# Kernel tuning notes

Hardware: AMD Instinct MI355X
Metric: run time of the kernel (lower is better)

Reference implementation:

```python
import jax, jax.numpy as jnp
import numpy as np

B, D = 8192, 128
MARGIN = 0.1
N_CLASSES, N_GROUPS = 64, 8


def setup_inputs() -> dict:
    key = jax.random.key(0)
    k1, k2, k3 = jax.random.split(key, 3)
    embeddings = jax.random.normal(k1, (B, D), dtype=jnp.float32)
    labels = jax.random.randint(k2, (B,), 0, N_CLASSES, dtype=jnp.int64)
    groups = jax.random.randint(k3, (B,), 0, N_GROUPS, dtype=jnp.int64)
    return {"embeddings": embeddings, "labels": labels, "groups": groups}


def reference(embeddings, labels, groups):
    # cosine metric: L2-normalize rows (torch F.normalize eps=1e-12)
    norm = jnp.maximum(jnp.linalg.norm(embeddings, axis=1, keepdims=True), 1e-12)
    x = embeddings / norm
    dist = 1.0 - jnp.matmul(x, x.T)                      # [B, B]

    n = embeddings.shape[0]
    eye = jnp.eye(n, dtype=bool)
    same_label = labels[:, None] == labels[None, :]       # [B, B]
    pos_mask = same_label & ~eye
    neg_mask = ~same_label
    neg_sg_mask = neg_mask & (groups[:, None] == groups[None, :])

    BIG = jnp.float32(1e9)
    # hardest positive per row (masked max), hardest negative per row (masked min)
    dist_ap = jnp.max(jnp.where(pos_mask, dist, -BIG), axis=1)
    dist_an_sg = jnp.min(jnp.where(neg_sg_mask, dist, BIG), axis=1)
    dist_an_all = jnp.min(jnp.where(neg_mask, dist, BIG), axis=1)

    has_pos = jnp.any(pos_mask, axis=1)
    has_neg_sg = jnp.any(neg_sg_mask, axis=1)
    has_neg = jnp.any(neg_mask, axis=1)

    # fallback: same-group negatives preferred, else any negative
    dist_an = jnp.where(has_neg_sg, dist_an_sg, dist_an_all)

    loss = jax.nn.relu(dist_ap - dist_an + MARGIN)        # [B]
    # original only averages strictly-positive losses over valid anchors
    include = has_pos & has_neg & (loss > 0)
    cnt = jnp.sum(include.astype(jnp.float32))
    total = jnp.sum(jnp.where(include, loss, 0.0))
    final = jnp.where(cnt > 0, total / jnp.maximum(cnt, 1.0), 0.0)
    final = jnp.where(jnp.isnan(final), 0.0, final)
    return final
```

## Files before the change

### kernel.cpp

```cpp
#include <hip/hip_runtime.h>
#include <math.h>

#define NB 8192
#define DK 128
#define TI 128
#define NTILES (NB / TI)
#define NBLK (NTILES * (NTILES + 1) / 2)
#define JT 64
#define NT (TI / JT)
#define BSTRH 136
#define NCOMB (NB / 256)

typedef __attribute__((ext_vector_type(8))) short short8;
typedef __attribute__((ext_vector_type(16))) float float16;

__device__ inline unsigned short f2bf(float f) {
    unsigned int x = __float_as_uint(f);
    unsigned int r = (x + 0x7fffu + ((x >> 16) & 1u)) >> 16;
    return (unsigned short)r;
}

__global__ void norm_kernel(const float* __restrict__ emb, const int* __restrict__ labels,
                            const int* __restrict__ groups, unsigned short* __restrict__ xnb,
                            int* __restrict__ meta, float* __restrict__ accum,
                            int* __restrict__ ticket) {
    int row  = blockIdx.x * 4 + (threadIdx.x >> 6);
    int lane = threadIdx.x & 63;
    float2 v = ((const float2*)(emb + (size_t)row * DK))[lane];
    float ss = v.x * v.x + v.y * v.y;
#pragma unroll
    for (int off = 32; off; off >>= 1) ss += __shfl_xor(ss, off, 64);
    float inv = 1.0f / fmaxf(sqrtf(ss), 1e-12f);
    ushort2 o;
    o.x = f2bf(v.x * inv);
    o.y = f2bf(v.y * inv);
    ((ushort2*)(xnb + (size_t)row * DK))[lane] = o;
    if (lane == 0) meta[row] = (labels[row] << 8) | groups[row];
    if (blockIdx.x == 0 && threadIdx.x == 0) {
        accum[0] = 0.0f; accum[1] = 0.0f; ticket[0] = 0;
    }
}

__global__ __launch_bounds__(256, 3) void mine_tri(
    const unsigned short* __restrict__ xnb, const int* __restrict__ meta,
    float2* __restrict__ part) {
    __shared__ unsigned short Bs[2][JT * BSTRH];

    int bid = blockIdx.x;
    int ti = 0;
    while (bid >= NTILES - ti) { bid -= NTILES - ti; ti++; }
    const int tj = ti + bid;

    const int tid  = threadIdx.x;
    const int w    = tid >> 6;
    const int lane = tid & 63;
    const int half = lane >> 5;
    const int l31  = lane & 31;
    const int i0    = ti * TI;
    const int jbase = tj * TI;
    const int irow  = i0 + w * 32;

    short8 afrag[8];
#pragma unroll
    for (int ks = 0; ks < 8; ks++)
        afrag[ks] = *(const short8*)(xnb + (size_t)(irow + l31) * DK + ks * 16 + half * 8);

    int metaI[16];
    float apn[16], anc[16];
#pragma unroll
    for (int reg = 0; reg < 16; reg++) {
        int r = (reg & 3) + 8 * (reg >> 2) + 4 * half;
        metaI[reg] = meta[irow + r];
        apn[reg] = -1e9f; anc[reg] = -1e9f;
    }
    float apnC[4], ancC[4];
#pragma unroll
    for (int q = 0; q < 4; q++) { apnC[q] = -1e9f; ancC[q] = -1e9f; }

#pragma unroll
    for (int s = 0; s < 4; s++) {
        int chunk = tid + s * 256;
        int row = chunk >> 4, k4 = chunk & 15;
        *(uint4*)&Bs[0][row * BSTRH + k4 * 8] =
            *(const uint4*)(xnb + (size_t)(jbase + row) * DK + k4 * 8);
    }
    __syncthreads();

#pragma unroll
    for (int jt = 0; jt < NT; jt++) {
        const int cur = jt & 1;
        const int j0  = jbase + jt * JT;

        uint4 pre[4];
        if (jt + 1 < NT) {
            const int j0n = j0 + JT;
#pragma unroll
            for (int s = 0; s < 4; s++) {
                int chunk = tid + s * 256;
                int row = chunk >> 4, k4 = chunk & 15;
                pre[s] = *(const uint4*)(xnb + (size_t)(j0n + row) * DK + k4 * 8);
            }
        }

        int mjc[2];
        mjc[0] = meta[j0 + l31];
        mjc[1] = meta[j0 + 32 + l31];

#pragma unroll
        for (int ct = 0; ct < 2; ct++) {
            float16 c;
#pragma unroll
            for (int e = 0; e < 16; e++) c[e] = 0.0f;

            const int bro = ct * 32 + l31;
#pragma unroll
            for (int ks = 0; ks < 8; ks++) {
                short8 b = *(const short8*)&Bs[cur][bro * BSTRH + ks * 16 + half * 8];
                c = __builtin_amdgcn_mfma_f32_32x32x16_bf16(afrag[ks], b, c, 0, 0, 0);
            }

            const int mj = mjc[ct];
            const int q  = jt * 2 + ct;
#pragma unroll
            for (int reg = 0; reg < 16; reg++) {
                float s = c[reg];
                int x = metaI[reg] ^ mj;
                bool sl = (unsigned)x < 0x100u;
                float t8 = s - 8.0f;
                float t  = sl ? t8 : s;
                float negt = -t;
                apn[reg] = fmaxf(apn[reg], negt);
                apnC[q]  = fmaxf(apnC[q],  negt);
                bool sg = (x & 0xFFu) == 0u;
                float t4 = t + 4.0f;
                float v  = sg ? t4 : t;
                anc[reg] = fmaxf(anc[reg], v);
                ancC[q]  = fmaxf(ancC[q],  v);
            }
        }

        if (jt + 1 < NT) {
#pragma unroll
            for (int s = 0; s < 4; s++) {
                int chunk = tid + s * 256;
                int row = chunk >> 4, k4 = chunk & 15;
                *(uint4*)&Bs[cur ^ 1][row * BSTRH + k4 * 8] = pre[s];
            }
        }
        __syncthreads();
    }

#pragma unroll
    for (int reg = 0; reg < 16; reg++) {
#pragma unroll
        for (int off = 16; off; off >>= 1) {
            apn[reg] = fmaxf(apn[reg], __shfl_xor(apn[reg], off, 64));
            anc[reg] = fmaxf(anc[reg], __shfl_xor(anc[reg], off, 64));
        }
    }
    if (l31 == 0) {
#pragma unroll
        for (int reg = 0; reg < 16; reg++) {
            int r = (reg & 3) + 8 * (reg >> 2) + 4 * half;
            float2 o; o.x = apn[reg]; o.y = anc[reg];
            part[(size_t)tj * NB + (irow + r)] = o;
        }
    }

    float* colred = (float*)&Bs[0][0];
#pragma unroll
    for (int q = 0; q < 4; q++) {
        apnC[q] = fmaxf(apnC[q], __shfl_xor(apnC[q], 32, 64));
        ancC[q] = fmaxf(ancC[q], __shfl_xor(ancC[q], 32, 64));
        if (half == 0) {
            colred[0 * 512 + w * 128 + q * 32 + l31] = apnC[q];
            colred[1 * 512 + w * 128 + q * 32 + l31] = ancC[q];
        }
    }
    __syncthreads();
    if (tid < 128 && ti != tj) {
        int e = tid;
        float ma = -1e9f, mn = -1e9f;
#pragma unroll
        for (int wv = 0; wv < 4; wv++) {
            ma = fmaxf(ma, colred[0 * 512 + wv * 128 + e]);
            mn = fmaxf(mn, colred[1 * 512 + wv * 128 + e]);
        }
        float2 o; o.x = ma; o.y = mn;
        part[(size_t)ti * NB + (jbase + e)] = o;
    }
}

__global__ void combine_kernel(const float2* __restrict__ part,
                               float* __restrict__ accum, int* __restrict__ ticket,
                               float* __restrict__ out) {
    int i = blockIdx.x * 256 + threadIdx.x;
    float a0 = -1e9f, a1 = -1e9f, a2 = -1e9f, a3 = -1e9f;
    float n0 = -1e9f, n1 = -1e9f, n2 = -1e9f, n3 = -1e9f;
#pragma unroll
    for (int s = 0; s < NTILES; s += 4) {
        float2 p0 = part[(size_t)(s + 0) * NB + i];
        float2 p1 = part[(size_t)(s + 1) * NB + i];
        float2 p2 = part[(size_t)(s + 2) * NB + i];
        float2 p3 = part[(size_t)(s + 3) * NB + i];
        a0 = fmaxf(a0, p0.x); n0 = fmaxf(n0, p0.y);
        a1 = fmaxf(a1, p1.x); n1 = fmaxf(n1, p1.y);
        a2 = fmaxf(a2, p2.x); n2 = fmaxf(n2, p2.y);
        a3 = fmaxf(a3, p3.x); n3 = fmaxf(n3, p3.y);
    }
    float apn = fmaxf(fmaxf(a0, a1), fmaxf(a2, a3));
    float anc = fmaxf(fmaxf(n0, n1), fmaxf(n2, n3));

    float anS = (anc > 2.0f) ? anc - 4.0f : anc;
    float loss = anS + apn - 7.9f;
    float inc = (loss > 0.0f) ? 1.0f : 0.0f;
    float val = inc * loss;

    __shared__ float ssum[4], scnt[4];
#pragma unroll
    for (int off = 32; off; off >>= 1) {
        val += __shfl_xor(val, off, 64);
        inc += __shfl_xor(inc, off, 64);
    }
    int wid = threadIdx.x >> 6, lane = threadIdx.x & 63;
    if (lane == 0) { ssum[wid] = val; scnt[wid] = inc; }
    __syncthreads();
    if (threadIdx.x == 0) {
        float s = 0.f, c = 0.f;
#pragma unroll
        for (int wv = 0; wv < 4; wv++) { s += ssum[wv]; c += scnt[wv]; }
        atomicAdd(&accum[0], s);
        atomicAdd(&accum[1], c);
        __threadfence();
        int old = atomicAdd(ticket, 1);
        if (old == gridDim.x - 1) {
            __threadfence();
            float total = __hip_atomic_load(&accum[0], __ATOMIC_RELAXED, __HIP_MEMORY_SCOPE_AGENT);
            float cnt   = __hip_atomic_load(&accum[1], __ATOMIC_RELAXED, __HIP_MEMORY_SCOPE_AGENT);
            float r = (cnt > 0.0f) ? total / fmaxf(cnt, 1.0f) : 0.0f;
            if (isnan(r)) r = 0.0f;
            out[0] = r;
        }
    }
}

extern "C" void kernel_launch(void* const* d_in, const int* in_sizes, int n_in,
                              void* d_out, int out_size, void* d_ws, size_t ws_size,
                              hipStream_t stream) {
    const float* emb  = (const float*)d_in[0];
    const int* labels = (const int*)d_in[1];
    const int* groups = (const int*)d_in[2];
    float* out = (float*)d_out;

    unsigned short* xnb = (unsigned short*)d_ws;
    int*    meta   = (int*)(xnb + (size_t)NB * DK);
    float2* part   = (float2*)(meta + NB);
    float*  accum  = (float*)(part + (size_t)NTILES * NB);
    int*    ticket = (int*)(accum + 2);

    norm_kernel<<<NB / 4, 256, 0, stream>>>(emb, labels, groups, xnb, meta, accum, ticket);
    mine_tri<<<NBLK, 256, 0, stream>>>(xnb, meta, part);
    combine_kernel<<<NCOMB, 256, 0, stream>>>(part, accum, ticket, out);
}
```

Before: 100.8 us.

## Switch symmetric mining to 128x256 strip tiles with sentinel-initialized partials

```diff
diff --git a/kernel.cpp b/kernel.cpp
--- a/kernel.cpp
+++ b/kernel.cpp
@@ -3,13 +3,14 @@
 
 #define NB 8192
 #define DK 128
-#define TI 128
-#define NTILES (NB / TI)
-#define NBLK (NTILES * (NTILES + 1) / 2)
+#define NTILES 64
+#define NCHUNK 32
+#define NBLK 1056
 #define JT 64
-#define NT (TI / JT)
+#define NT 4
 #define BSTRH 136
-#define NCOMB (NB / 256)
+#define NSLOT 96
+#define SENT -1.7e38f
 
 typedef __attribute__((ext_vector_type(8))) short short8;
 typedef __attribute__((ext_vector_type(16))) float float16;
@@ -22,8 +23,8 @@
 
 __global__ void norm_kernel(const float* __restrict__ emb, const int* __restrict__ labels,
                             const int* __restrict__ groups, unsigned short* __restrict__ xnb,
-                            int* __restrict__ meta, float* __restrict__ accum,
-                            int* __restrict__ ticket) {
+                            int* __restrict__ meta, float2* __restrict__ part,
+                            float* __restrict__ accum, int* __restrict__ ticket) {
     int row  = blockIdx.x * 4 + (threadIdx.x >> 6);
     int lane = threadIdx.x & 63;
     float2 v = ((const float2*)(emb + (size_t)row * DK))[lane];
@@ -36,29 +37,38 @@
     o.y = f2bf(v.y * inv);
     ((ushort2*)(xnb + (size_t)row * DK))[lane] = o;
     if (lane == 0) meta[row] = (labels[row] << 8) | groups[row];
+
+    size_t g = (size_t)blockIdx.x * 256 + threadIdx.x;
+    float2 snt; snt.x = SENT; snt.y = SENT;
+    part[g] = snt;
+    if (g < (size_t)NSLOT * NB - 524288) part[g + 524288] = snt;
+
     if (blockIdx.x == 0 && threadIdx.x == 0) {
         accum[0] = 0.0f; accum[1] = 0.0f; ticket[0] = 0;
     }
 }
 
-__global__ __launch_bounds__(256, 3) void mine_tri(
+__global__ __launch_bounds__(256, 3) void mine_strip(
     const unsigned short* __restrict__ xnb, const int* __restrict__ meta,
     float2* __restrict__ part) {
     __shared__ unsigned short Bs[2][JT * BSTRH];
+    __shared__ float colred[2][4][8][32];
 
     int bid = blockIdx.x;
-    int ti = 0;
-    while (bid >= NTILES - ti) { bid -= NTILES - ti; ti++; }
-    const int tj = ti + bid;
+    int u = 0;
+    while (bid >= 2 * (NCHUNK - u)) { bid -= 2 * (NCHUNK - u); u++; }
+    const int cnt = NCHUNK - u;
+    const int sel = (bid >= cnt) ? 1 : 0;
+    const int ti  = 2 * u + sel;
+    const int c   = u + (sel ? bid - cnt : bid);
 
     const int tid  = threadIdx.x;
     const int w    = tid >> 6;
     const int lane = tid & 63;
     const int half = lane >> 5;
     const int l31  = lane & 31;
-    const int i0    = ti * TI;
-    const int jbase = tj * TI;
-    const int irow  = i0 + w * 32;
+    const int jbase = c * 256;
+    const int irow  = ti * 128 + w * 32;
 
     short8 afrag[8];
 #pragma unroll
@@ -73,9 +83,6 @@
         metaI[reg] = meta[irow + r];
         apn[reg] = -1e9f; anc[reg] = -1e9f;
     }
-    float apnC[4], ancC[4];
-#pragma unroll
-    for (int q = 0; q < 4; q++) { apnC[q] = -1e9f; ancC[q] = -1e9f; }
 
 #pragma unroll
     for (int s = 0; s < 4; s++) {
@@ -106,36 +113,47 @@
         mjc[0] = meta[j0 + l31];
         mjc[1] = meta[j0 + 32 + l31];
 
+        float apnC2[2], ancC2[2];
 #pragma unroll
         for (int ct = 0; ct < 2; ct++) {
-            float16 c;
-#pragma unroll
-            for (int e = 0; e < 16; e++) c[e] = 0.0f;
+            float16 cc;
+#pragma unroll
+            for (int e = 0; e < 16; e++) cc[e] = 0.0f;
 
             const int bro = ct * 32 + l31;
 #pragma unroll
             for (int ks = 0; ks < 8; ks++) {
                 short8 b = *(const short8*)&Bs[cur][bro * BSTRH + ks * 16 + half * 8];
-                c = __builtin_amdgcn_mfma_f32_32x32x16_bf16(afrag[ks], b, c, 0, 0, 0);
+                cc = __builtin_amdgcn_mfma_f32_32x32x16_bf16(afrag[ks], b, cc, 0, 0, 0);
             }
 
             const int mj = mjc[ct];
-            const int q  = jt * 2 + ct;
+            float ca = -1e9f, cn = -1e9f;
 #pragma unroll
             for (int reg = 0; reg < 16; reg++) {
-                float s = c[reg];
+                float s = cc[reg];
                 int x = metaI[reg] ^ mj;
                 bool sl = (unsigned)x < 0x100u;
                 float t8 = s - 8.0f;
                 float t  = sl ? t8 : s;
-                float negt = -t;
-                apn[reg] = fmaxf(apn[reg], negt);
-                apnC[q]  = fmaxf(apnC[q],  negt);
+                apn[reg] = fmaxf(apn[reg], -t);
+                ca = fmaxf(ca, -t);
                 bool sg = (x & 0xFFu) == 0u;
                 float t4 = t + 4.0f;
                 float v  = sg ? t4 : t;
                 anc[reg] = fmaxf(anc[reg], v);
-                ancC[q]  = fmaxf(ancC[q],  v);
+                cn = fmaxf(cn, v);
+            }
+            apnC2[ct] = ca; ancC2[ct] = cn;
+        }
+
+#pragma unroll
+        for (int ct2 = 0; ct2 < 2; ct2++) {
+            float a = fmaxf(apnC2[ct2], __shfl_xor(apnC2[ct2], 32, 64));
+            float n = fmaxf(ancC2[ct2], __shfl_xor(ancC2[ct2], 32, 64));
+            if (half == 0) {
+                colred[0][w][jt * 2 + ct2][l31] = a;
+                colred[1][w][jt * 2 + ct2][l31] = n;
             }
         }
 
@@ -163,42 +181,31 @@
         for (int reg = 0; reg < 16; reg++) {
             int r = (reg & 3) + 8 * (reg >> 2) + 4 * half;
             float2 o; o.x = apn[reg]; o.y = anc[reg];
-            part[(size_t)tj * NB + (irow + r)] = o;
-        }
-    }
-
-    float* colred = (float*)&Bs[0][0];
-#pragma unroll
-    for (int q = 0; q < 4; q++) {
-        apnC[q] = fmaxf(apnC[q], __shfl_xor(apnC[q], 32, 64));
-        ancC[q] = fmaxf(ancC[q], __shfl_xor(ancC[q], 32, 64));
-        if (half == 0) {
-            colred[0 * 512 + w * 128 + q * 32 + l31] = apnC[q];
-            colred[1 * 512 + w * 128 + q * 32 + l31] = ancC[q];
-        }
-    }
-    __syncthreads();
-    if (tid < 128 && ti != tj) {
-        int e = tid;
+            part[(size_t)(64 + c) * NB + (irow + r)] = o;
+        }
+    }
+
+    {
+        int q = tid >> 5, l = tid & 31;
         float ma = -1e9f, mn = -1e9f;
 #pragma unroll
         for (int wv = 0; wv < 4; wv++) {
-            ma = fmaxf(ma, colred[0 * 512 + wv * 128 + e]);
-            mn = fmaxf(mn, colred[1 * 512 + wv * 128 + e]);
+            ma = fmaxf(ma, colred[0][wv][q][l]);
+            mn = fmaxf(mn, colred[1][wv][q][l]);
         }
         float2 o; o.x = ma; o.y = mn;
-        part[(size_t)ti * NB + (jbase + e)] = o;
+        part[(size_t)ti * NB + (jbase + tid)] = o;
     }
 }
 
 __global__ void combine_kernel(const float2* __restrict__ part,
                                float* __restrict__ accum, int* __restrict__ ticket,
                                float* __restrict__ out) {
-    int i = blockIdx.x * 256 + threadIdx.x;
-    float a0 = -1e9f, a1 = -1e9f, a2 = -1e9f, a3 = -1e9f;
-    float n0 = -1e9f, n1 = -1e9f, n2 = -1e9f, n3 = -1e9f;
-#pragma unroll
-    for (int s = 0; s < NTILES; s += 4) {
+    int i = blockIdx.x * 64 + threadIdx.x;
+    float a0 = -3e38f, a1 = -3e38f, a2 = -3e38f, a3 = -3e38f;
+    float n0 = -3e38f, n1 = -3e38f, n2 = -3e38f, n3 = -3e38f;
+#pragma unroll
+    for (int s = 0; s < NSLOT; s += 4) {
         float2 p0 = part[(size_t)(s + 0) * NB + i];
         float2 p1 = part[(size_t)(s + 1) * NB + i];
         float2 p2 = part[(size_t)(s + 2) * NB + i];
@@ -216,21 +223,14 @@
     float inc = (loss > 0.0f) ? 1.0f : 0.0f;
     float val = inc * loss;
 
-    __shared__ float ssum[4], scnt[4];
 #pragma unroll
     for (int off = 32; off; off >>= 1) {
         val += __shfl_xor(val, off, 64);
         inc += __shfl_xor(inc, off, 64);
     }
-    int wid = threadIdx.x >> 6, lane = threadIdx.x & 63;
-    if (lane == 0) { ssum[wid] = val; scnt[wid] = inc; }
-    __syncthreads();
     if (threadIdx.x == 0) {
-        float s = 0.f, c = 0.f;
-#pragma unroll
-        for (int wv = 0; wv < 4; wv++) { s += ssum[wv]; c += scnt[wv]; }
-        atomicAdd(&accum[0], s);
-        atomicAdd(&accum[1], c);
+        atomicAdd(&accum[0], val);
+        atomicAdd(&accum[1], inc);
         __threadfence();
         int old = atomicAdd(ticket, 1);
         if (old == gridDim.x - 1) {
@@ -255,10 +255,10 @@
     unsigned short* xnb = (unsigned short*)d_ws;
     int*    meta   = (int*)(xnb + (size_t)NB * DK);
     float2* part   = (float2*)(meta + NB);
-    float*  accum  = (float*)(part + (size_t)NTILES * NB);
+    float*  accum  = (float*)(part + (size_t)NSLOT * NB);
     int*    ticket = (int*)(accum + 2);
 
-    norm_kernel<<<NB / 4, 256, 0, stream>>>(emb, labels, groups, xnb, meta, accum, ticket);
-    mine_tri<<<NBLK, 256, 0, stream>>>(xnb, meta, part);
-    combine_kernel<<<NCOMB, 256, 0, stream>>>(part, accum, ticket, out);
-}
+    norm_kernel<<<NB / 4, 256, 0, stream>>>(emb, labels, groups, xnb, meta, part, accum, ticket);
+    mine_strip<<<NBLK, 256, 0, stream>>>(xnb, meta, part);
+    combine_kernel<<<128, 64, 0, stream>>>(part, accum, ticket, out);
+}
```

Result: slower. 162.1 us (+60.8%).
